# Kernel tuning notes

Hardware: AMD Instinct MI355X
Metric: run time of the kernel (lower is better)

The kernel has to match this reference:

```python
import jax, jax.numpy as jnp
import numpy as np


def setup_inputs() -> dict:
    key = jax.random.key(0)
    k1, k2 = jax.random.split(key)
    B, T, F, H = 32, 2048, 400, 1152
    x = jax.random.normal(k1, (B, T, F), dtype=jnp.float32)
    # fused gate weights (F*kernel_window, 3*H); small init like keras 'uniform'
    W = jax.random.normal(k2, (2 * F, 3 * H), dtype=jnp.float32) * 0.05
    b = jnp.zeros((3 * H,), dtype=jnp.float32)
    h0 = jnp.zeros((B, H), dtype=jnp.float32)
    return {"x": x, "W": W, "b": b, "h0": h0}


def reference(x, W, b, h0):
    """QRNN with 'fo' pooling, kernel_window=2, keep_fastai_bug=True, inference.

    Per timestep (as in QRNNCell_.call):
      merged_t = [x_t, x_{t-1}]                      (x_{-1} = 0)
      z, f, o  = split(merged_t @ W + b, 3)
      z = tanh(z); f = sigmoid(f); o = sigmoid(o)
      h_t = z*f + (1-f)*h_{t-1}   (fastai-bug variant; h is carried state)
      c_t = o*h_t                 (cell output at step t)
    Returns the full output sequence c: [B, T, H].
    """
    B, T, F = x.shape
    # previous-timestep inputs (kernel_window=2): shift right, zero-pad t=0
    x_prev = jnp.concatenate([jnp.zeros((B, 1, F), x.dtype), x[:, :-1]], axis=1)
    merged = jnp.concatenate([x, x_prev], axis=-1)            # [B, T, 2F]
    logits = jnp.einsum('btf,fg->btg', merged, W) + b          # [B, T, 3H]
    z, f, o = jnp.split(logits, 3, axis=-1)
    z = jnp.tanh(z)
    f = jax.nn.sigmoid(f)
    o = jax.nn.sigmoid(o)

    def step(h_prev, gates):
        zt, ft, ot = gates
        h_t = zt * ft + (1.0 - ft) * h_prev
        return h_t, ot * h_t

    # scan over time: [T, B, H]
    _, c = jax.lax.scan(step, h0,
                        (z.transpose(1, 0, 2), f.transpose(1, 0, 2), o.transpose(1, 0, 2)))
    return c.transpose(1, 0, 2)                                # [B, T, H]
```

## Files before the change

### kernel.cpp

```cpp
#include <hip/hip_runtime.h>

#define BB 32
#define TT 2048
#define FF 400
#define HH 1152
#define MM 65536
#define NN 3456
#define KK 800
#define MT2 256
#define NT 27
#define KTL 25
#define CH 64
#define CL 32

typedef __attribute__((ext_vector_type(8))) short short8;
typedef __attribute__((ext_vector_type(4))) float f32x4;
typedef _Float16 hx4 __attribute__((ext_vector_type(4)));
typedef float f2 __attribute__((ext_vector_type(2)));

__device__ __forceinline__ unsigned short f2bf(float f) {
  union { float f; unsigned u; } v; v.f = f;
  unsigned r = v.u + 0x7FFFu + ((v.u >> 16) & 1u);
  return (unsigned short)(r >> 16);
}

__device__ __forceinline__ void async16(void* lds, const void* g) {
  __builtin_amdgcn_global_load_lds((const __attribute__((address_space(1))) void*)g,
                                   (__attribute__((address_space(3))) void*)lds, 16, 0, 0);
}

__device__ __forceinline__ size_t quadOff(int mt, int ntS, int wr, int wc,
                                          int mr, int nr, int kg, int l15) {
  return ((((size_t)(mt * 9 + ntS) * 2 + wr) * 2 + wc) * 32 + mr * 4 + nr) * 256
         + (size_t)(kg * 16 + l15) * 4;
}

__global__ __launch_bounds__(256) void pack_W_k(const float* __restrict__ W,
                                                unsigned short* __restrict__ Wws) {
  const int nt = blockIdx.x, kt = blockIdx.y;
  for (int c = threadIdx.x; c < 512; c += 256) {
    const int kg = c >> 7, n = c & 127;
    const int g = nt * 128 + n;
    const int k0 = kt * 32 + kg * 8;
    short8 o;
#pragma unroll
    for (int j = 0; j < 8; ++j) o[j] = (short)f2bf(W[(size_t)(k0 + j) * NN + g]);
    *(short8*)(Wws + ((size_t)(nt * KTL + kt) * 512 + c) * 8) = o;
  }
}

__global__ __launch_bounds__(256) void pack_A_k(const float* __restrict__ x,
                                                unsigned short* __restrict__ Aws) {
  const int mt = blockIdx.x, kt = blockIdx.y;
  for (int c = threadIdx.x; c < 1024; c += 256) {
    const int kg = c >> 8, mm = c & 255;
    const int m = mt * 256 + mm;
    const int b = m >> 11, t = m & 2047;
    const int k = kt * 32 + kg * 8;
    short8 o;
    const float* src = nullptr;
    if (k < FF) src = x + (size_t)(b * TT + t) * FF + k;
    else if (t > 0) src = x + (size_t)(b * TT + t - 1) * FF + (k - FF);
    if (src) {
      f32x4 v0 = *(const f32x4*)(src);
      f32x4 v1 = *(const f32x4*)(src + 4);
#pragma unroll
      for (int j = 0; j < 4; ++j) o[j] = (short)f2bf(v0[j]);
#pragma unroll
      for (int j = 0; j < 4; ++j) o[4 + j] = (short)f2bf(v1[j]);
    } else {
#pragma unroll
      for (int j = 0; j < 8; ++j) o[j] = 0;
    }
    *(short8*)(Aws + ((size_t)(mt * KTL + kt) * 1024 + c) * 8) = o;
  }
}

__global__ __launch_bounds__(256, 2) void gemm_k(const unsigned short* __restrict__ Aws,
                                                 const unsigned short* __restrict__ Wws,
                                                 const float* __restrict__ bias,
                                                 _Float16* __restrict__ Zh,
                                                 _Float16* __restrict__ Fh,
                                                 _Float16* __restrict__ Oh) {
  __shared__ unsigned short As[3][8192];
  __shared__ unsigned short Bs[3][4096];

  const int bid = blockIdx.x;
  const int xcd = bid & 7;
  const int local = bid >> 3;
  const int ng = local / 288;
  const int r0 = local - ng * 288;
  const int mtl = r0 / 9;
  const int nti = r0 - mtl * 9;
  const int mt = xcd * 32 + mtl;
  const int nt = ng * 9 + nti;

  const int tid = threadIdx.x;
  const int lane = tid & 63, w = tid >> 6;
  const int wr = w >> 1, wc = w & 1;
  const int l15 = lane & 15, kg = lane >> 4;

  const unsigned short* ga = Aws + (size_t)mt * KTL * 8192;
  const unsigned short* gb = Wws + (size_t)nt * KTL * 4096;

  f32x4 acc[8][4] = {};
  short8 a0[8], b0[4], a1[8], b1[4];

  const int aoff = kg * 256 + wr * 128;
  const int boff = kg * 128 + wc * 64;

#define STAGE(tt)                                                        \
  do {                                                                   \
    const int _bi = (tt) % 3;                                            \
    const unsigned short* _a = ga + (size_t)(tt) * 8192;                 \
    const unsigned short* _b = gb + (size_t)(tt) * 4096;                 \
    async16(&As[_bi][tid * 8], _a + tid * 8);                            \
    async16(&As[_bi][2048 + tid * 8], _a + 2048 + tid * 8);              \
    async16(&As[_bi][4096 + tid * 8], _a + 4096 + tid * 8);              \
    async16(&As[_bi][6144 + tid * 8], _a + 6144 + tid * 8);              \
    async16(&Bs[_bi][tid * 8], _b + tid * 8);                            \
    async16(&Bs[_bi][2048 + tid * 8], _b + 2048 + tid * 8);              \
  } while (0)

#define READF(AF, BF, bufi)                                                        \
  do {                                                                             \
    _Pragma("unroll")                                                              \
    for (int mr = 0; mr < 8; ++mr)                                                 \
      AF[mr] = *(const short8*)&As[bufi][(size_t)(aoff + mr * 16 + l15) * 8];      \
    _Pragma("unroll")                                                              \
    for (int nr = 0; nr < 4; ++nr)                                                 \
      BF[nr] = *(const short8*)&Bs[bufi][(size_t)(boff + nr * 16 + l15) * 8];      \
  } while (0)

#define MFMAC(AF, BF)                                                              \
  do {                                                                             \
    __builtin_amdgcn_s_setprio(1);                                                 \
    _Pragma("unroll")                                                              \
    for (int mr = 0; mr < 8; ++mr)                                                 \
      _Pragma("unroll")                                                            \
      for (int nr = 0; nr < 4; ++nr)                                               \
        acc[mr][nr] = __builtin_amdgcn_mfma_f32_16x16x32_bf16(AF[mr], BF[nr],      \
                                                              acc[mr][nr], 0, 0, 0); \
    __builtin_amdgcn_s_setprio(0);                                                 \
  } while (0)

  STAGE(0);
  STAGE(1);
  asm volatile("s_waitcnt vmcnt(6)" ::: "memory");
  asm volatile("s_barrier" ::: "memory");
  READF(a0, b0, 0);

#pragma unroll 1
  for (int t = 0; t < KTL - 1; t += 2) {
    asm volatile("s_waitcnt vmcnt(0)" ::: "memory");
    asm volatile("s_barrier" ::: "memory");
    if (t + 2 < KTL) STAGE(t + 2);
    READF(a1, b1, (t + 1) % 3);
    MFMAC(a0, b0);

    asm volatile("s_waitcnt vmcnt(0)" ::: "memory");
    asm volatile("s_barrier" ::: "memory");
    if (t + 3 < KTL) STAGE(t + 3);
    if (t + 2 < KTL) READF(a0, b0, (t + 2) % 3);
    MFMAC(a1, b1);
  }
  MFMAC(a0, b0);

#undef STAGE
#undef READF
#undef MFMAC

  const int sector = ng;
  const int ntS = nti;
  _Float16* __restrict__ dst = (sector == 0) ? Zh : ((sector == 1) ? Fh : Oh);
  const int gbase = nt * 128 + wc * 64 + l15;
  const size_t wavebase = (((size_t)(mt * 9 + ntS) * 2 + wr) * 2 + wc) * 8192 + (size_t)lane * 4;
#pragma unroll
  for (int nr = 0; nr < 4; ++nr) {
    const float bv = bias[gbase + nr * 16];
#pragma unroll
    for (int mr = 0; mr < 8; ++mr) {
      f32x4 v = acc[mr][nr];
      hx4 hv;
#pragma unroll
      for (int rr = 0; rr < 4; ++rr) {
        float xv = v[rr] + bv;
        float s;
        if (sector == 0) {
          float e = __expf(2.0f * xv);
          s = 1.0f - 2.0f / (e + 1.0f);
        } else {
          s = 1.0f / (1.0f + __expf(-xv));
        }
        hv[rr] = (_Float16)s;
      }
      __builtin_nontemporal_store(hv, (hx4*)(dst + wavebase + (size_t)(mr * 4 + nr) * 256));
    }
  }
}

__global__ __launch_bounds__(256) void scan1_k(const _Float16* __restrict__ Zh,
                                               const _Float16* __restrict__ Fh,
                                               f2* __restrict__ PQ) {
  const int bid = blockIdx.x;
  const int b = bid / 288;
  const int rem = bid - b * 288;
  const int hb = rem >> 5, cp = rem & 31;
  const int tid = threadIdx.x;
  const int hloc = tid & 127, sub = tid >> 7;
  const int ch = cp * 2 + sub;
  const int ntS = hb, wc = hloc >> 6, nr = (hloc >> 4) & 3, l15 = hloc & 15;
  const int tm = ch >> 3, wr = (ch >> 2) & 1, mrh = ch & 3;
  const int mt = b * 8 + tm;

  float P = 1.f, Q = 0.f;
#pragma unroll
  for (int mi = 0; mi < 2; ++mi) {
#pragma unroll
    for (int kg = 0; kg < 4; ++kg) {
      const size_t off = quadOff(mt, ntS, wr, wc, mrh * 2 + mi, nr, kg, l15);
      hx4 z = __builtin_nontemporal_load((const hx4*)(Zh + off));
      hx4 f = __builtin_nontemporal_load((const hx4*)(Fh + off));
#pragma unroll
      for (int s = 0; s < 4; ++s) {
        float fv = (float)f[s], a = 1.f - fv;
        P *= a;
        Q = a * Q + fv * (float)z[s];
      }
    }
  }
  f2 o; o[0] = P; o[1] = Q;
  PQ[((size_t)b * CH + ch) * HH + hb * 128 + hloc] = o;
}

__global__ __launch_bounds__(256) void scan2_k(const f2* __restrict__ PQ,
                                               const float* __restrict__ h0,
                                               float* __restrict__ Hs) {
  const int idx = blockIdx.x * 256 + threadIdx.x;
  const int b = idx / HH, h = idx - b * HH;
  float cur = h0[b * HH + h];
#pragma unroll 4
  for (int c = 0; c < CH; ++c) {
    Hs[((size_t)b * CH + c) * HH + h] = cur;
    f2 pq = PQ[((size_t)b * CH + c) * HH + h];
    cur = pq[0] * cur + pq[1];
  }
}

__global__ __launch_bounds__(256) void scan3_k(const _Float16* __restrict__ Zh,
                                               const _Float16* __restrict__ Fh,
                                               const _Float16* __restrict__ Oh,
                                               const float* __restrict__ Hs,
                                               float* __restrict__ Out) {
  __shared__ float buf[64 * 132];
  const int bid = blockIdx.x;
  const int b = bid / 288;
  const int rem = bid - b * 288;
  const int hb = rem >> 5, cp = rem & 31;
  const int tid = threadIdx.x;
  const int hloc = tid & 127, sub = tid >> 7;
  const int ch = cp * 2 + sub;
  const int h = hb * 128 + hloc;
  const int ntS = hb, wc = hloc >> 6, nr = (hloc >> 4) & 3, l15 = hloc & 15;
  const int tm = ch >> 3, wr = (ch >> 2) & 1, mrh = ch & 3;
  const int mt = b * 8 + tm;

  float hcur = Hs[((size_t)b * CH + ch) * HH + h];
#pragma unroll
  for (int mi = 0; mi < 2; ++mi) {
#pragma unroll
    for (int kg = 0; kg < 4; ++kg) {
      const size_t off = quadOff(mt, ntS, wr, wc, mrh * 2 + mi, nr, kg, l15);
      hx4 z = __builtin_nontemporal_load((const hx4*)(Zh + off));
      hx4 f = __builtin_nontemporal_load((const hx4*)(Fh + off));
      hx4 o = __builtin_nontemporal_load((const hx4*)(Oh + off));
#pragma unroll
      for (int s = 0; s < 4; ++s) {
        hcur = fmaf((float)f[s], (float)z[s] - hcur, hcur);
        buf[(sub * 32 + mi * 16 + kg * 4 + s) * 132 + hloc] = (float)o[s] * hcur;
      }
    }
  }
  __syncthreads();
  const int lane32 = tid & 31, grp = tid >> 5;
  float* outb = Out + (size_t)(b * TT + cp * 64) * HH + hb * 128 + lane32 * 4;
#pragma unroll
  for (int rr = 0; rr < 8; ++rr) {
    const int row = grp * 8 + rr;
    f32x4 v = *(const f32x4*)&buf[row * 132 + lane32 * 4];
    __builtin_nontemporal_store(v, (f32x4*)(outb + (size_t)row * HH));
  }
}

extern "C" void kernel_launch(void* const* d_in, const int* in_sizes, int n_in,
                              void* d_out, int out_size, void* d_ws, size_t ws_size,
                              hipStream_t stream) {
  const float* x    = (const float*)d_in[0];
  const float* W    = (const float*)d_in[1];
  const float* bias = (const float*)d_in[2];
  const float* h0   = (const float*)d_in[3];
  float* Out = (float*)d_out;
  char* ws = (char*)d_ws;

  const size_t A_BYTES  = (size_t)MT2 * KTL * 16384;
  const size_t W_BYTES  = (size_t)NT * KTL * 8192;
  const size_t G_BYTES  = (size_t)MM * HH * 2;
  const size_t PQ_BYTES = (size_t)BB * CH * HH * 8;
  unsigned short* Aws = (unsigned short*)ws;
  unsigned short* Wws = (unsigned short*)(ws + A_BYTES);
  _Float16* Zh = (_Float16*)(ws + A_BYTES + W_BYTES);
  _Float16* Fh = (_Float16*)(ws + A_BYTES + W_BYTES + G_BYTES);
  _Float16* Oh = (_Float16*)(ws + A_BYTES + W_BYTES + 2 * G_BYTES);
  f2* PQ = (f2*)(ws + A_BYTES + W_BYTES + 3 * G_BYTES);
  float* Hs = (float*)(ws + A_BYTES + W_BYTES + 3 * G_BYTES + PQ_BYTES);
  (void)ws_size; (void)in_sizes; (void)n_in; (void)out_size;

  pack_W_k<<<dim3(NT, KTL), 256, 0, stream>>>(W, Wws);
  pack_A_k<<<dim3(MT2, KTL), 256, 0, stream>>>(x, Aws);
  gemm_k<<<MT2 * NT, 256, 0, stream>>>(Aws, Wws, bias, Zh, Fh, Oh);
  scan1_k<<<BB * 9 * 32, 256, 0, stream>>>(Zh, Fh, PQ);
  scan2_k<<<BB * HH / 256, 256, 0, stream>>>(PQ, h0, Hs);
  scan3_k<<<BB * 9 * 32, 256, 0, stream>>>(Zh, Fh, Oh, Hs, Out);
}
```

Measured before the change: 662.7 us.

## Load GEMM fragments directly from global memory into registers, dropping LDS staging

Removes the triple-buffered LDS staging (global_load_lds plus barriers) in the GEMM and instead has each wave load its MFMA fragments straight from the pre-swizzled global buffers into registers, double-buffered across k-tiles. This removes the LDS traffic and block-wide barriers. The cost is that each A and B tile is now fetched from global/L2 separately by every wave that uses it, and load latency is hidden only by register double buffering.

```diff
diff --git a/kernel.cpp b/kernel.cpp
--- a/kernel.cpp
+++ b/kernel.cpp
@@ -22,11 +22,6 @@
   union { float f; unsigned u; } v; v.f = f;
   unsigned r = v.u + 0x7FFFu + ((v.u >> 16) & 1u);
   return (unsigned short)(r >> 16);
-}
-
-__device__ __forceinline__ void async16(void* lds, const void* g) {
-  __builtin_amdgcn_global_load_lds((const __attribute__((address_space(1))) void*)g,
-                                   (__attribute__((address_space(3))) void*)lds, 16, 0, 0);
 }
 
 __device__ __forceinline__ size_t quadOff(int mt, int ntS, int wr, int wc,
@@ -82,9 +77,6 @@
                                                  _Float16* __restrict__ Zh,
                                                  _Float16* __restrict__ Fh,
                                                  _Float16* __restrict__ Oh) {
-  __shared__ unsigned short As[3][8192];
-  __shared__ unsigned short Bs[3][4096];
-
   const int bid = blockIdx.x;
   const int xcd = bid & 7;
   const int local = bid >> 3;
@@ -100,36 +92,22 @@
   const int wr = w >> 1, wc = w & 1;
   const int l15 = lane & 15, kg = lane >> 4;
 
-  const unsigned short* ga = Aws + (size_t)mt * KTL * 8192;
-  const unsigned short* gb = Wws + (size_t)nt * KTL * 4096;
+  const unsigned short* ga = Aws + (size_t)mt * KTL * 8192
+                             + (size_t)(kg * 256 + wr * 128 + l15) * 8;
+  const unsigned short* gb = Wws + (size_t)nt * KTL * 4096
+                             + (size_t)(kg * 128 + wc * 64 + l15) * 8;
 
   f32x4 acc[8][4] = {};
   short8 a0[8], b0[4], a1[8], b1[4];
 
-  const int aoff = kg * 256 + wr * 128;
-  const int boff = kg * 128 + wc * 64;
-
-#define STAGE(tt)                                                        \
-  do {                                                                   \
-    const int _bi = (tt) % 3;                                            \
-    const unsigned short* _a = ga + (size_t)(tt) * 8192;                 \
-    const unsigned short* _b = gb + (size_t)(tt) * 4096;                 \
-    async16(&As[_bi][tid * 8], _a + tid * 8);                            \
-    async16(&As[_bi][2048 + tid * 8], _a + 2048 + tid * 8);              \
-    async16(&As[_bi][4096 + tid * 8], _a + 4096 + tid * 8);              \
-    async16(&As[_bi][6144 + tid * 8], _a + 6144 + tid * 8);              \
-    async16(&Bs[_bi][tid * 8], _b + tid * 8);                            \
-    async16(&Bs[_bi][2048 + tid * 8], _b + 2048 + tid * 8);              \
-  } while (0)
-
-#define READF(AF, BF, bufi)                                                        \
-  do {                                                                             \
-    _Pragma("unroll")                                                              \
-    for (int mr = 0; mr < 8; ++mr)                                                 \
-      AF[mr] = *(const short8*)&As[bufi][(size_t)(aoff + mr * 16 + l15) * 8];      \
-    _Pragma("unroll")                                                              \
-    for (int nr = 0; nr < 4; ++nr)                                                 \
-      BF[nr] = *(const short8*)&Bs[bufi][(size_t)(boff + nr * 16 + l15) * 8];      \
+#define LOADT(AF, BF, tt)                                                    \
+  do {                                                                       \
+    const unsigned short* _a = ga + (size_t)(tt) * 8192;                     \
+    const unsigned short* _b = gb + (size_t)(tt) * 4096;                     \
+    _Pragma("unroll")                                                        \
+    for (int mr = 0; mr < 8; ++mr) AF[mr] = *(const short8*)(_a + mr * 128); \
+    _Pragma("unroll")                                                        \
+    for (int nr = 0; nr < 4; ++nr) BF[nr] = *(const short8*)(_b + nr * 128); \
   } while (0)
 
 #define MFMAC(AF, BF)                                                              \
@@ -144,30 +122,19 @@
     __builtin_amdgcn_s_setprio(0);                                                 \
   } while (0)
 
-  STAGE(0);
-  STAGE(1);
-  asm volatile("s_waitcnt vmcnt(6)" ::: "memory");
-  asm volatile("s_barrier" ::: "memory");
-  READF(a0, b0, 0);
+  LOADT(a0, b0, 0);
+  LOADT(a1, b1, 1);
 
 #pragma unroll 1
   for (int t = 0; t < KTL - 1; t += 2) {
-    asm volatile("s_waitcnt vmcnt(0)" ::: "memory");
-    asm volatile("s_barrier" ::: "memory");
-    if (t + 2 < KTL) STAGE(t + 2);
-    READF(a1, b1, (t + 1) % 3);
     MFMAC(a0, b0);
-
-    asm volatile("s_waitcnt vmcnt(0)" ::: "memory");
-    asm volatile("s_barrier" ::: "memory");
-    if (t + 3 < KTL) STAGE(t + 3);
-    if (t + 2 < KTL) READF(a0, b0, (t + 2) % 3);
+    if (t + 2 < KTL) LOADT(a0, b0, t + 2);
     MFMAC(a1, b1);
+    if (t + 3 < KTL) LOADT(a1, b1, t + 3);
   }
   MFMAC(a0, b0);
 
-#undef STAGE
-#undef READF
+#undef LOADT
 #undef MFMAC
 
   const int sector = ng;
```

Result: faster. 616.6 us (-7.0%).
